# Performance work log

Hardware: AMD Instinct MI355X
Metric: run time of the kernel (lower is better)

## Reference

```python
import jax, jax.numpy as jnp
import numpy as np

N = 50000      # nodes
D = 256        # input_features
K = 64         # hiddens (per-head out dim)
H = 8          # nheads
O = 64         # outputs
E = 1600000    # edges
ALPHA = 0.2    # leaky-relu negative slope


def setup_inputs() -> dict:
    key = jax.random.key(0)
    ks = jax.random.split(key, 8)
    x = jax.random.normal(ks[0], (N, D), dtype=jnp.float32)
    edges = jax.random.randint(ks[1], (2, E), 0, N, dtype=jnp.int64)
    layer_W = jax.random.normal(ks[2], (D, D), dtype=jnp.float32) * (1.0 / np.sqrt(D))
    layer_b = jnp.zeros((D,), dtype=jnp.float32)
    heads_W = jax.random.normal(ks[3], (H, D, K), dtype=jnp.float32) * (1.0 / np.sqrt(D))
    heads_a = jax.random.normal(ks[4], (H, 2 * K), dtype=jnp.float32) * 0.1
    end_W = jax.random.normal(ks[5], (H * K, O), dtype=jnp.float32) * (1.0 / np.sqrt(H * K))
    end_a = jax.random.normal(ks[6], (2 * O,), dtype=jnp.float32) * 0.1
    return {"x": x, "edges": edges, "layer_W": layer_W, "layer_b": layer_b,
            "heads_W": heads_W, "heads_a": heads_a, "end_W": end_W, "end_a": end_a}


def _gat_layer(x, W, a, src, dst):
    # x: [N, Din], W: [Din, Dout], a: [2*Dout]
    h = x @ W                                    # [N, Dout]
    k = h.shape[1]
    # a . [h_src || h_dst] == (h @ a_src)[src] + (h @ a_dst)[dst]  (cheap: project then gather scalars)
    s = (h @ a[:k])[src] + (h @ a[k:])[dst]      # [E]
    e = jax.nn.leaky_relu(s, ALPHA)
    # numerically-stable segment softmax over edges grouped by destination node
    m = jax.ops.segment_max(e, dst, num_segments=N)        # [N]
    w = jnp.exp(e - m[dst])                                # [E]
    denom = jax.ops.segment_sum(w, dst, num_segments=N)    # [N]
    attn = w / (denom[dst] + 1e-16)                        # [E]
    out = jax.ops.segment_sum(attn[:, None] * h[src], dst, num_segments=N)  # [N, Dout]
    return jax.nn.elu(out)


def reference(x, edges, layer_W, layer_b, heads_W, heads_a, end_W, end_a):
    src, dst = edges[0], edges[1]
    x = x @ layer_W + layer_b                    # nn.Linear(input_features, input_features)
    # multi-head sparse attention, concat over heads -> [N, H*K]
    hcat = jnp.concatenate(
        [_gat_layer(x, heads_W[i], heads_a[i], src, dst) for i in range(H)], axis=1)
    out = _gat_layer(hcat, end_W, end_a, src, dst)  # [N, O]
    return jax.nn.softmax(out, axis=1)
```

## Files before the change

### kernel.cpp

```cpp
#include <hip/hip_runtime.h>
#include <hip/hip_fp16.h>
#include <math.h>

#define NN 50000
#define DD 256
#define KK 64
#define HH 8
#define OO 64
#define EE 1600000
#define LRELU_ALPHA 0.2f
#define HK 512
#define NX 640
#define N3 80

typedef __attribute__((ext_vector_type(8))) short short8;
typedef __attribute__((ext_vector_type(4))) float floatx4;
typedef __attribute__((ext_vector_type(4))) unsigned int uintx4;

__device__ inline void bsplit(float f, unsigned short& h, unsigned short& l) {
    unsigned u = __float_as_uint(f);
    h = (unsigned short)(u >> 16);
    float fh = __uint_as_float(u & 0xffff0000u);
    l = (unsigned short)(__float_as_uint(f - fh) >> 16);
}

__device__ inline void fmamix2(float& a0, float& a1, unsigned int pk, float w) {
    asm("v_fma_mix_f32 %0, %2, %3, %0 op_sel:[0,0,0] op_sel_hi:[1,0,0]\n\t"
        "v_fma_mix_f32 %1, %2, %3, %1 op_sel:[1,0,0] op_sel_hi:[1,0,0]"
        : "+v"(a0), "+v"(a1)
        : "v"(pk), "v"(w));
}

__global__ void pack_heads_kernel(const float* __restrict__ hw, float* __restrict__ Bp) {
    int t = blockIdx.x * 256 + threadIdx.x;
    if (t >= HH * DD * KK) return;
    int h = t >> 14;
    int r = t & 16383;
    int d = r >> 6;
    int k = r & 63;
    Bp[d * HK + h * KK + k] = hw[t];
}

__global__ void bias_pack_kernel(const float* __restrict__ b, const float* __restrict__ Bp,
                                 float* __restrict__ bc) {
    int c = blockIdx.x * 256 + threadIdx.x;
    if (c >= HK) return;
    float s = 0.f;
    for (int d = 0; d < DD; d++) s += b[d] * Bp[d * HK + c];
    bc[c] = s;
}

__global__ void build_wext_kernel(const float* __restrict__ Wc, const float* __restrict__ heads_a,
                                  unsigned short* __restrict__ Th, unsigned short* __restrict__ Tl) {
    int t = blockIdx.x * 256 + threadIdx.x;
    int col = t >> 8, d = t & 255;
    if (col >= NX) return;
    float v = 0.f;
    if (col < HK) {
        v = Wc[d * HK + col];
    } else if (col < HK + 8) {
        int h = col - HK;
        for (int k = 0; k < 64; k++) v += Wc[d * HK + h * 64 + k] * heads_a[h * 128 + k];
    } else if (col < HK + 16) {
        int h = col - HK - 8;
        for (int k = 0; k < 64; k++) v += Wc[d * HK + h * 64 + k] * heads_a[h * 128 + 64 + k];
    }
    unsigned short hi, lo;
    bsplit(v, hi, lo);
    Th[(size_t)col * DD + d] = hi;
    Tl[(size_t)col * DD + d] = lo;
}

__global__ void bias_ext_kernel(const float* __restrict__ bc, const float* __restrict__ heads_a,
                                float* __restrict__ be) {
    int c = blockIdx.x * 256 + threadIdx.x;
    if (c >= NX) return;
    float v = 0.f;
    if (c < HK) v = bc[c];
    else if (c < HK + 8) {
        int h = c - HK;
        for (int k = 0; k < 64; k++) v += bc[h * 64 + k] * heads_a[h * 128 + k];
    } else if (c < HK + 16) {
        int h = c - HK - 8;
        for (int k = 0; k < 64; k++) v += bc[h * 64 + k] * heads_a[h * 128 + 64 + k];
    }
    be[c] = v;
}

__global__ void build_eext_kernel(const float* __restrict__ eW, const float* __restrict__ ea,
                                  unsigned short* __restrict__ Th, unsigned short* __restrict__ Tl) {
    int t = blockIdx.x * 256 + threadIdx.x;
    int col = t >> 9, k = t & 511;
    if (col >= N3) return;
    float v = 0.f;
    if (col < OO) v = eW[(size_t)k * OO + col];
    else if (col == OO) { for (int j = 0; j < OO; j++) v += eW[(size_t)k * OO + j] * ea[j]; }
    else if (col == OO + 1) { for (int j = 0; j < OO; j++) v += eW[(size_t)k * OO + j] * ea[64 + j]; }
    unsigned short hi, lo;
    bsplit(v, hi, lo);
    Th[(size_t)col * HK + k] = hi;
    Tl[(size_t)col * HK + k] = lo;
}

__global__ void split_x_kernel(const float* __restrict__ x, unsigned short* __restrict__ xh,
                               unsigned short* __restrict__ xl) {
    int t = blockIdx.x * 256 + threadIdx.x;
    if (t >= NN * 64) return;
    float4 v = ((const float4*)x)[t];
    ushort4 vh, vl;
    bsplit(v.x, vh.x, vl.x);
    bsplit(v.y, vh.y, vl.y);
    bsplit(v.z, vh.z, vl.z);
    bsplit(v.w, vh.w, vl.w);
    ((ushort4*)xh)[t] = vh;
    ((ushort4*)xl)[t] = vl;
}

#define GM 128
#define GN 128
#define GKT 16
__global__ __launch_bounds__(256) void sgemm128_kernel(
    const float* __restrict__ A, const float* __restrict__ B,
    const float* __restrict__ bias, float* __restrict__ C,
    int M, int N, int K)
{
    __shared__ float As[GKT][GM + 4];
    __shared__ float Bs[GKT][GN + 4];
    int tid = threadIdx.x;
    int row0 = blockIdx.y * GM, col0 = blockIdx.x * GN;
    int tx = tid & 15, ty = tid >> 4;
    int ar = tid >> 1;
    int ac0 = (tid & 1) * 8;
    float acc[8][8] = {};
    for (int k0 = 0; k0 < K; k0 += GKT) {
#pragma unroll
        for (int i = 0; i < 2; i++) {
            int gr = row0 + ar;
            int gc = k0 + ac0 + i * 4;
            float4 v = make_float4(0.f, 0.f, 0.f, 0.f);
            if (gr < M) v = *(const float4*)&A[(size_t)gr * K + gc];
            As[ac0 + i * 4 + 0][ar] = v.x;
            As[ac0 + i * 4 + 1][ar] = v.y;
            As[ac0 + i * 4 + 2][ar] = v.z;
            As[ac0 + i * 4 + 3][ar] = v.w;
        }
#pragma unroll
        for (int i = 0; i < 2; i++) {
            int idx = tid + i * 256;
            int br = idx >> 5;
            int bc = (idx & 31) * 4;
            float4 v = make_float4(0.f, 0.f, 0.f, 0.f);
            int gc = col0 + bc;
            if (gc < N) v = *(const float4*)&B[(size_t)(k0 + br) * N + gc];
            *(float4*)&Bs[br][bc] = v;
        }
        __syncthreads();
#pragma unroll
        for (int k = 0; k < GKT; k++) {
            float4 a0 = *(const float4*)&As[k][ty * 4];
            float4 a1 = *(const float4*)&As[k][64 + ty * 4];
            float4 b0 = *(const float4*)&Bs[k][tx * 4];
            float4 b1 = *(const float4*)&Bs[k][64 + tx * 4];
            float av[8] = {a0.x, a0.y, a0.z, a0.w, a1.x, a1.y, a1.z, a1.w};
            float bv[8] = {b0.x, b0.y, b0.z, b0.w, b1.x, b1.y, b1.z, b1.w};
#pragma unroll
            for (int i = 0; i < 8; i++)
#pragma unroll
                for (int j = 0; j < 8; j++) acc[i][j] += av[i] * bv[j];
        }
        __syncthreads();
    }
#pragma unroll
    for (int i = 0; i < 8; i++) {
        int gr = row0 + (i < 4 ? ty * 4 + i : 64 + ty * 4 + i - 4);
        if (gr >= M) continue;
#pragma unroll
        for (int j = 0; j < 8; j++) {
            int gc = col0 + (j < 4 ? tx * 4 + j : 64 + tx * 4 + j - 4);
            if (gc >= N) continue;
            float v = acc[i][j];
            if (bias) v += bias[gc];
            C[(size_t)gr * N + gc] = v;
        }
    }
}

#define LDA 40
__global__ __launch_bounds__(256) void mfma_gemm1_kernel(
    const unsigned short* __restrict__ xh, const unsigned short* __restrict__ xl,
    const unsigned short* __restrict__ BhT, const unsigned short* __restrict__ BlT,
    const float* __restrict__ bias_ext,
    __half* __restrict__ Hh, float* __restrict__ ssrc_n, float* __restrict__ sdst_n)
{
    __shared__ unsigned short AhL[128 * LDA];
    __shared__ unsigned short AlL[128 * LDA];
    __shared__ unsigned short BhL[128 * LDA];
    __shared__ unsigned short BlL[128 * LDA];
    int tid = threadIdx.x, widx = tid >> 6, lane = tid & 63;
    int row0 = blockIdx.y * 128, col0 = blockIdx.x * 128;
    int wrow = (widx >> 1) * 64, wcol = (widx & 1) * 64;
    int lrow = lane & 15, lq = lane >> 4;
    int sr = tid >> 1;
    int sc = (tid & 1) * 16;
    int gr = row0 + sr;
    size_t abase = (gr < NN) ? (size_t)gr * DD : 0;
    size_t bbase = (size_t)(col0 + sr) * DD;
    floatx4 acc[4][4] = {};
    uint4 pah0, pah1, pal0, pal1, pbh0, pbh1, pbl0, pbl1;
    {
        size_t ab = abase + sc, bb = bbase + sc;
        pah0 = *(const uint4*)&xh[ab];   pah1 = *(const uint4*)&xh[ab + 8];
        pal0 = *(const uint4*)&xl[ab];   pal1 = *(const uint4*)&xl[ab + 8];
        pbh0 = *(const uint4*)&BhT[bb];  pbh1 = *(const uint4*)&BhT[bb + 8];
        pbl0 = *(const uint4*)&BlT[bb];  pbl1 = *(const uint4*)&BlT[bb + 8];
    }
    for (int k0 = 0; k0 < DD; k0 += 32) {
        *(uint4*)&AhL[sr * LDA + sc]     = pah0;
        *(uint4*)&AhL[sr * LDA + sc + 8] = pah1;
        *(uint4*)&AlL[sr * LDA + sc]     = pal0;
        *(uint4*)&AlL[sr * LDA + sc + 8] = pal1;
        *(uint4*)&BhL[sr * LDA + sc]     = pbh0;
        *(uint4*)&BhL[sr * LDA + sc + 8] = pbh1;
        *(uint4*)&BlL[sr * LDA + sc]     = pbl0;
        *(uint4*)&BlL[sr * LDA + sc + 8] = pbl1;
        __syncthreads();
        if (k0 + 32 < DD) {
            size_t ab = abase + k0 + 32 + sc, bb = bbase + k0 + 32 + sc;
            pah0 = *(const uint4*)&xh[ab];   pah1 = *(const uint4*)&xh[ab + 8];
            pal0 = *(const uint4*)&xl[ab];   pal1 = *(const uint4*)&xl[ab + 8];
            pbh0 = *(const uint4*)&BhT[bb];  pbh1 = *(const uint4*)&BhT[bb + 8];
            pbl0 = *(const uint4*)&BlT[bb];  pbl1 = *(const uint4*)&BlT[bb + 8];
        }
        short8 ah[4], al[4], bh[4], bl[4];
#pragma unroll
        for (int mi = 0; mi < 4; mi++) {
            int r = wrow + mi * 16 + lrow;
            ah[mi] = *(const short8*)&AhL[r * LDA + lq * 8];
            al[mi] = *(const short8*)&AlL[r * LDA + lq * 8];
        }
#pragma unroll
        for (int ni = 0; ni < 4; ni++) {
            int c = wcol + ni * 16 + lrow;
            bh[ni] = *(const short8*)&BhL[c * LDA + lq * 8];
            bl[ni] = *(const short8*)&BlL[c * LDA + lq * 8];
        }
#pragma unroll
        for (int mi = 0; mi < 4; mi++)
#pragma unroll
            for (int ni = 0; ni < 4; ni++) {
                acc[mi][ni] = __builtin_amdgcn_mfma_f32_16x16x32_bf16(al[mi], bh[ni], acc[mi][ni], 0, 0, 0);
                acc[mi][ni] = __builtin_amdgcn_mfma_f32_16x16x32_bf16(ah[mi], bl[ni], acc[mi][ni], 0, 0, 0);
                acc[mi][ni] = __builtin_amdgcn_mfma_f32_16x16x32_bf16(ah[mi], bh[ni], acc[mi][ni], 0, 0, 0);
            }
        __syncthreads();
    }
#pragma unroll
    for (int mi = 0; mi < 4; mi++)
#pragma unroll
        for (int ni = 0; ni < 4; ni++)
#pragma unroll
            for (int r = 0; r < 4; r++) {
                int grow = row0 + wrow + mi * 16 + lq * 4 + r;
                int gcol = col0 + wcol + ni * 16 + lrow;
                if (grow < NN && gcol < HK + 16) {
                    float v = acc[mi][ni][r] + bias_ext[gcol];
                    if (gcol < HK)
                        Hh[(size_t)grow * HK + gcol] = __float2half_rn(v);
                    else if (gcol < HK + 8)
                        ssrc_n[(size_t)grow * 8 + (gcol - HK)] = v;
                    else
                        sdst_n[(size_t)grow * 8 + (gcol - HK - 8)] = v;
                }
            }
}

__global__ __launch_bounds__(256) void mfma_gemm3_kernel(
    const unsigned short* __restrict__ hch, const unsigned short* __restrict__ hcl,
    const unsigned short* __restrict__ BhT, const unsigned short* __restrict__ BlT,
    __half* __restrict__ h2, float* __restrict__ s2src, float* __restrict__ s2dst)
{
    __shared__ unsigned short AhL[64 * LDA];
    __shared__ unsigned short AlL[64 * LDA];
    __shared__ unsigned short BhL[N3 * LDA];
    __shared__ unsigned short BlL[N3 * LDA];
    int tid = threadIdx.x, widx = tid >> 6, lane = tid & 63;
    int row0 = blockIdx.x * 64;
    int wrow = widx * 16;
    int lrow = lane & 15, lq = lane >> 4;
    int sr = tid >> 2;
    int sc = (tid & 3) * 8;
    int gr = row0 + sr;
    size_t abase = (gr < NN) ? (size_t)gr * HK : 0;
    int bidx0 = tid;
    int br0 = bidx0 >> 2, bc0 = (bidx0 & 3) * 8;
    int bidx1 = tid + 256;
    bool b1ok = (bidx1 < N3 * 4);
    int br1 = bidx1 >> 2, bc1 = (bidx1 & 3) * 8;
    floatx4 acc[5] = {};
    uint4 pa0, pa1, pb0h, pb0l, pb1h, pb1l;
    {
        pa0 = *(const uint4*)&hch[abase + sc];
        pa1 = *(const uint4*)&hcl[abase + sc];
        pb0h = *(const uint4*)&BhT[(size_t)br0 * HK + bc0];
        pb0l = *(const uint4*)&BlT[(size_t)br0 * HK + bc0];
        if (b1ok) {
            pb1h = *(const uint4*)&BhT[(size_t)br1 * HK + bc1];
            pb1l = *(const uint4*)&BlT[(size_t)br1 * HK + bc1];
        }
    }
    for (int k0 = 0; k0 < HK; k0 += 32) {
        *(uint4*)&AhL[sr * LDA + sc] = pa0;
        *(uint4*)&AlL[sr * LDA + sc] = pa1;
        *(uint4*)&BhL[br0 * LDA + bc0] = pb0h;
        *(uint4*)&BlL[br0 * LDA + bc0] = pb0l;
        if (b1ok) {
            *(uint4*)&BhL[br1 * LDA + bc1] = pb1h;
            *(uint4*)&BlL[br1 * LDA + bc1] = pb1l;
        }
        __syncthreads();
        if (k0 + 32 < HK) {
            size_t ab = abase + k0 + 32 + sc;
            pa0 = *(const uint4*)&hch[ab];
            pa1 = *(const uint4*)&hcl[ab];
            pb0h = *(const uint4*)&BhT[(size_t)br0 * HK + k0 + 32 + bc0];
            pb0l = *(const uint4*)&BlT[(size_t)br0 * HK + k0 + 32 + bc0];
            if (b1ok) {
                pb1h = *(const uint4*)&BhT[(size_t)br1 * HK + k0 + 32 + bc1];
                pb1l = *(const uint4*)&BlT[(size_t)br1 * HK + k0 + 32 + bc1];
            }
        }
        short8 ah, al, bh[5], bl[5];
        int r = wrow + lrow;
        ah = *(const short8*)&AhL[r * LDA + lq * 8];
        al = *(const short8*)&AlL[r * LDA + lq * 8];
#pragma unroll
        for (int ni = 0; ni < 5; ni++) {
            int c = ni * 16 + lrow;
            bh[ni] = *(const short8*)&BhL[c * LDA + lq * 8];
            bl[ni] = *(const short8*)&BlL[c * LDA + lq * 8];
        }
#pragma unroll
        for (int ni = 0; ni < 5; ni++) {
            acc[ni] = __builtin_amdgcn_mfma_f32_16x16x32_bf16(al, bh[ni], acc[ni], 0, 0, 0);
            acc[ni] = __builtin_amdgcn_mfma_f32_16x16x32_bf16(ah, bl[ni], acc[ni], 0, 0, 0);
            acc[ni] = __builtin_amdgcn_mfma_f32_16x16x32_bf16(ah, bh[ni], acc[ni], 0, 0, 0);
        }
        __syncthreads();
    }
#pragma unroll
    for (int ni = 0; ni < 5; ni++)
#pragma unroll
        for (int r = 0; r < 4; r++) {
            int grow = row0 + wrow + lq * 4 + r;
            int gcol = ni * 16 + lrow;
            if (grow < NN) {
                float v = acc[ni][r];
                if (gcol < OO) h2[(size_t)grow * OO + gcol] = __float2half_rn(v);
                else if (gcol == OO) s2src[grow] = v;
                else if (gcol == OO + 1) s2dst[grow] = v;
            }
        }
}

__global__ void hist_kernel(const int* __restrict__ dst, int* __restrict__ deg) {
    int t = blockIdx.x * 256 + threadIdx.x;
    if (t < EE) atomicAdd(&deg[dst[t]], 1);
}

__global__ void scan1_kernel(const int* __restrict__ deg, int* __restrict__ part,
                             int* __restrict__ bsum) {
    __shared__ int ws_[4];
    int i = blockIdx.x * 256 + threadIdx.x;
    int lane = threadIdx.x & 63, wv = threadIdx.x >> 6;
    int v = (i < NN) ? deg[i] : 0;
    int x = v;
#pragma unroll
    for (int d = 1; d < 64; d <<= 1) {
        int t = __shfl_up(x, d, 64);
        if (lane >= d) x += t;
    }
    if (lane == 63) ws_[wv] = x;
    __syncthreads();
    int add = 0;
    for (int k = 0; k < wv; k++) add += ws_[k];
    x += add;
    if (i < NN) part[i] = x;
    if (threadIdx.x == 255) bsum[blockIdx.x] = x;
}

__global__ void scan2_kernel(int* __restrict__ bsum, int nb) {
    __shared__ int ws_[4];
    int tid = threadIdx.x;
    int lane = tid & 63, wv = tid >> 6;
    int v = (tid < nb) ? bsum[tid] : 0;
    int x = v;
#pragma unroll
    for (int d = 1; d < 64; d <<= 1) {
        int t = __shfl_up(x, d, 64);
        if (lane >= d) x += t;
    }
    if (lane == 63) ws_[wv] = x;
    __syncthreads();
    int add = 0;
    for (int k = 0; k < wv; k++) add += ws_[k];
    x += add;
    if (tid < nb) bsum[tid] = x;
}

__global__ void scan3_kernel(const int* __restrict__ deg, const int* __restrict__ part,
                             const int* __restrict__ bsum, int* __restrict__ offs,
                             int* __restrict__ cursor) {
    int i = blockIdx.x * 256 + threadIdx.x;
    if (i >= NN) return;
    int carry = blockIdx.x ? bsum[blockIdx.x - 1] : 0;
    int incl = part[i] + carry;
    offs[i + 1] = incl;
    cursor[i] = incl - deg[i];
    if (i == 0) offs[0] = 0;
}

__global__ void scatter_kernel(const int* __restrict__ src, const int* __restrict__ dst,
                               int* __restrict__ cursor, int* __restrict__ ssorted) {
    int t = blockIdx.x * 256 + threadIdx.x;
    if (t < EE) {
        int d = dst[t];
        int pos = atomicAdd(&cursor[d], 1);
        ssorted[pos] = src[t];
    }
}

#define APE 4
__global__ __launch_bounds__(256) void agg_heads_kernel(
    const __half* __restrict__ Hh, const float* __restrict__ ssrc_n,
    const float* __restrict__ sdst_n, const int* __restrict__ offs,
    const int* __restrict__ ssorted,
    unsigned short* __restrict__ hch, unsigned short* __restrict__ hcl)
{
    __shared__ int2 sSW[4][64];
    int wv = threadIdx.x >> 6, lane = threadIdx.x & 63;
    int n = blockIdx.x * 4 + wv;
    if (n >= NN) return;
    int beg = offs[n], deg = offs[n + 1] - beg;
    int eg = lane >> 3, hh = lane & 7;
    float acc[8] = {};
    float den = 0.f;
    float sd = sdst_n[(size_t)n * 8 + hh];
    for (int c0 = 0; c0 < deg; c0 += 8) {
        int jj = c0 + eg;
        int s = 0;
        float wgt = 0.f;
        if (jj < deg) {
            s = ssorted[beg + jj];
            float sv = ssrc_n[(size_t)s * 8 + hh] + sd;
            float e = (sv >= 0.f) ? sv : LRELU_ALPHA * sv;
            wgt = __expf(e);
        }
        den += wgt;
        sSW[wv][lane] = make_int2(s, __float_as_int(wgt));
        int ec = min(8, deg - c0);
#pragma unroll
        for (int base = 0; base < 8; base += APE) {
            if (base >= ec) break;
            uint4 vb[APE];
            float wb[APE];
#pragma unroll
            for (int p = 0; p < APE; p++) {
                int2 t2 = sSW[wv][(base + p) * 8 + (lane >> 3)];
                wb[p] = __int_as_float(t2.y);
                vb[p] = *(const uint4*)&Hh[((size_t)t2.x << 9) + lane * 8];
            }
#pragma unroll
            for (int p = 0; p < APE; p++) {
                fmamix2(acc[0], acc[1], vb[p].x, wb[p]);
                fmamix2(acc[2], acc[3], vb[p].y, wb[p]);
                fmamix2(acc[4], acc[5], vb[p].z, wb[p]);
                fmamix2(acc[6], acc[7], vb[p].w, wb[p]);
            }
        }
    }
    den += __shfl_xor(den, 8, 64);
    den += __shfl_xor(den, 16, 64);
    den += __shfl_xor(den, 32, 64);
    float denf = __shfl(den, lane >> 3, 64);
    float inv = 1.f / (denf + 1e-16f);
    unsigned int phw[4], plw[4];
#pragma unroll
    for (int j = 0; j < 4; j++) {
        float r0 = acc[2 * j] * inv, r1 = acc[2 * j + 1] * inv;
        r0 = (r0 > 0.f) ? r0 : (__expf(r0) - 1.f);
        r1 = (r1 > 0.f) ? r1 : (__expf(r1) - 1.f);
        unsigned short h0, l0, h1, l1;
        bsplit(r0, h0, l0);
        bsplit(r1, h1, l1);
        phw[j] = (unsigned)h0 | ((unsigned)h1 << 16);
        plw[j] = (unsigned)l0 | ((unsigned)l1 << 16);
    }
    size_t o = (size_t)n * HK + lane * 8;
    uintx4 vph, vpl;
    vph.x = phw[0]; vph.y = phw[1]; vph.z = phw[2]; vph.w = phw[3];
    vpl.x = plw[0]; vpl.y = plw[1]; vpl.z = plw[2]; vpl.w = plw[3];
    __builtin_nontemporal_store(vph, (uintx4*)&hch[o]);
    __builtin_nontemporal_store(vpl, (uintx4*)&hcl[o]);
}

#define APW 4
__global__ __launch_bounds__(256) void agg_final_kernel(
    const __half* __restrict__ h2, const float* __restrict__ s2src,
    const float* __restrict__ s2dst, const int* __restrict__ offs,
    const int* __restrict__ ssorted, float* __restrict__ out)
{
    __shared__ int2 sSW[4][64];
    int wv = threadIdx.x >> 6, lane = threadIdx.x & 63;
    int n = blockIdx.x * 4 + wv;
    if (n >= NN) return;
    int beg = offs[n], deg = offs[n + 1] - beg;
    int g = lane >> 3, q = lane & 7;
    float acc[8] = {};
    float den = 0.f;
    float sd = (deg > 0) ? s2dst[n] : 0.f;
    for (int c0 = 0; c0 < deg; c0 += 64) {
        int jj = c0 + lane;
        int s = 0;
        float wgt = 0.f;
        if (jj < deg) {
            s = ssorted[beg + jj];
            float sv = s2src[s] + sd;
            float e = (sv >= 0.f) ? sv : LRELU_ALPHA * sv;
            wgt = __expf(e);
        }
        den += wgt;
        sSW[wv][lane] = make_int2(s, __float_as_int(wgt));
        int clen = min(64, deg - c0);
        int nst = (clen + 7) >> 3;
        for (int base = 0; base < nst; base += APW) {
            uint4 vb[APW];
            float wb[APW];
#pragma unroll
            for (int p2 = 0; p2 < APW; p2++) {
                int st = base + p2;
                int sj = 0;
                float ww = 0.f;
                if (st < nst) {
                    int2 t2 = sSW[wv][st * 8 + g];
                    sj = t2.x;
                    ww = __int_as_float(t2.y);
                }
                wb[p2] = ww;
                vb[p2] = *(const uint4*)&h2[(size_t)sj * OO + q * 8];
            }
#pragma unroll
            for (int p2 = 0; p2 < APW; p2++) {
                fmamix2(acc[0], acc[1], vb[p2].x, wb[p2]);
                fmamix2(acc[2], acc[3], vb[p2].y, wb[p2]);
                fmamix2(acc[4], acc[5], vb[p2].z, wb[p2]);
                fmamix2(acc[6], acc[7], vb[p2].w, wb[p2]);
            }
        }
    }
#pragma unroll
    for (int off = 32; off; off >>= 1) den += __shfl_xor(den, off, 64);
#pragma unroll
    for (int f = 0; f < 8; f++) {
        acc[f] += __shfl_xor(acc[f], 8, 64);
        acc[f] += __shfl_xor(acc[f], 16, 64);
        acc[f] += __shfl_xor(acc[f], 32, 64);
    }
    float inv = 1.f / (den + 1e-16f);
    float r[8];
#pragma unroll
    for (int f = 0; f < 8; f++) {
        float v = acc[f] * inv;
        r[f] = (v > 0.f) ? v : (__expf(v) - 1.f);
    }
    float mm = r[0];
#pragma unroll
    for (int f = 1; f < 8; f++) mm = fmaxf(mm, r[f]);
#pragma unroll
    for (int off = 1; off < 8; off <<= 1) mm = fmaxf(mm, __shfl_xor(mm, off, 64));
    float p[8], sum = 0.f;
#pragma unroll
    for (int f = 0; f < 8; f++) { p[f] = __expf(r[f] - mm); sum += p[f]; }
#pragma unroll
    for (int off = 1; off < 8; off <<= 1) sum += __shfl_xor(sum, off, 64);
    float is = 1.f / sum;
    if (g == 0) {
        float4 o0 = make_float4(p[0] * is, p[1] * is, p[2] * is, p[3] * is);
        float4 o1 = make_float4(p[4] * is, p[5] * is, p[6] * is, p[7] * is);
        *(float4*)&out[(size_t)n * OO + q * 8] = o0;
        *(float4*)&out[(size_t)n * OO + q * 8 + 4] = o1;
    }
}

extern "C" void kernel_launch(void* const* d_in, const int* in_sizes, int n_in,
                              void* d_out, int out_size, void* d_ws, size_t ws_size,
                              hipStream_t stream) {
    const float* x       = (const float*)d_in[0];
    const int*   edges   = (const int*)d_in[1];
    const float* layer_W = (const float*)d_in[2];
    const float* layer_b = (const float*)d_in[3];
    const float* heads_W = (const float*)d_in[4];
    const float* heads_a = (const float*)d_in[5];
    const float* end_W   = (const float*)d_in[6];
    const float* end_a   = (const float*)d_in[7];
    float* out = (float*)d_out;

    const int* src = edges;
    const int* dst = edges + EE;

    char* ws = (char*)d_ws;
    size_t wsp = 0;
    auto alloc = [&](size_t bytes) -> void* {
        void* r = ws + wsp;
        wsp += (bytes + 255) & ~(size_t)255;
        return r;
    };
    __half* Hh    = (__half*)alloc((size_t)NN * HK * 2);
    unsigned short* hch = (unsigned short*)alloc((size_t)NN * HK * 2);
    unsigned short* hcl = (unsigned short*)alloc((size_t)NN * HK * 2);
    __half* h2    = (__half*)alloc((size_t)NN * OO * 2);
    float* Bp    = (float*)alloc((size_t)DD * HK * 4);
    float* Wc    = (float*)alloc((size_t)DD * HK * 4);
    float* bc    = (float*)alloc((size_t)HK * 4);
    unsigned short* WexthT = (unsigned short*)alloc((size_t)NX * DD * 2);
    unsigned short* WextlT = (unsigned short*)alloc((size_t)NX * DD * 2);
    unsigned short* eexthT = (unsigned short*)alloc((size_t)N3 * HK * 2);
    unsigned short* eextlT = (unsigned short*)alloc((size_t)N3 * HK * 2);
    float* bias_ext = (float*)alloc((size_t)NX * 4);
    float* ssrc_n = (float*)alloc((size_t)NN * 8 * 4);
    float* sdst_n = (float*)alloc((size_t)NN * 8 * 4);
    float* s2src = (float*)alloc((size_t)NN * 4);
    float* s2dst = (float*)alloc((size_t)NN * 4);
    int* deg     = (int*)alloc((size_t)NN * 4);
    int* offs    = (int*)alloc((size_t)(NN + 1) * 4);
    int* cursor  = (int*)alloc((size_t)NN * 4);
    int* part    = (int*)alloc((size_t)NN * 4);
    int* bsum    = (int*)alloc((size_t)256 * 4);
    int* ssorted = (int*)alloc((size_t)EE * 4);

    unsigned short* xh = hch;
    unsigned short* xl = hcl;

    const int NB = (NN + 255) / 256;

    (void)hipMemsetAsync(deg, 0, (size_t)NN * 4, stream);

    pack_heads_kernel<<<(HH * DD * KK + 255) / 256, 256, 0, stream>>>(heads_W, Bp);
    bias_pack_kernel<<<2, 256, 0, stream>>>(layer_b, Bp, bc);
    sgemm128_kernel<<<dim3(HK / GN, DD / GM), 256, 0, stream>>>(
        layer_W, Bp, nullptr, Wc, DD, HK, DD);
    build_wext_kernel<<<(NX * DD + 255) / 256, 256, 0, stream>>>(Wc, heads_a, WexthT, WextlT);
    bias_ext_kernel<<<(NX + 255) / 256, 256, 0, stream>>>(bc, heads_a, bias_ext);
    build_eext_kernel<<<(N3 * HK + 255) / 256, 256, 0, stream>>>(end_W, end_a, eexthT, eextlT);
    split_x_kernel<<<(NN * 64 + 255) / 256, 256, 0, stream>>>(x, xh, xl);

    mfma_gemm1_kernel<<<dim3(NX / 128, (NN + 127) / 128), 256, 0, stream>>>(
        xh, xl, WexthT, WextlT, bias_ext, Hh, ssrc_n, sdst_n);

    hist_kernel<<<(EE + 255) / 256, 256, 0, stream>>>(dst, deg);
    scan1_kernel<<<NB, 256, 0, stream>>>(deg, part, bsum);
    scan2_kernel<<<1, 256, 0, stream>>>(bsum, NB);
    scan3_kernel<<<NB, 256, 0, stream>>>(deg, part, bsum, offs, cursor);
    scatter_kernel<<<(EE + 255) / 256, 256, 0, stream>>>(src, dst, cursor, ssorted);

    agg_heads_kernel<<<(NN + 3) / 4, 256, 0, stream>>>(
        Hh, ssrc_n, sdst_n, offs, ssorted, hch, hcl);

    mfma_gemm3_kernel<<<(NN + 63) / 64, 256, 0, stream>>>(
        hch, hcl, eexthT, eextlT, h2, s2src, s2dst);

    agg_final_kernel<<<(NN + 3) / 4, 256, 0, stream>>>(h2, s2src, s2dst, offs, ssorted, out);
}
```

Baseline: 802.5 us.

## Split head aggregation into head-pair passes with head-group-major feature layout

GEMM1 now writes the per-head features in a head-pair-major layout, [4 groups][N][2 heads][64]. The head aggregation kernel launches four times as many blocks, each covering one head pair, so each gathered source row is a contiguous 256-byte chunk. The working set per pass is smaller, which is meant to improve cache hit rates on the random gathers. In exchange, the CSR offsets, indices and softmax scores are re-read four times, and cross-lane shuffle reductions are added over the four edge sub-groups, which do redundant work.

After: 780.4 us. 1.03x faster.

```diff
diff --git a/kernel.cpp b/kernel.cpp
--- a/kernel.cpp
+++ b/kernel.cpp
@@ -12,6 +12,7 @@
 #define HK 512
 #define NX 640
 #define N3 80
+#define NGB 12500
 
 typedef __attribute__((ext_vector_type(8))) short short8;
 typedef __attribute__((ext_vector_type(4))) float floatx4;
@@ -190,7 +191,7 @@
     const unsigned short* __restrict__ xh, const unsigned short* __restrict__ xl,
     const unsigned short* __restrict__ BhT, const unsigned short* __restrict__ BlT,
     const float* __restrict__ bias_ext,
-    __half* __restrict__ Hh, float* __restrict__ ssrc_n, float* __restrict__ sdst_n)
+    __half* __restrict__ Hh2, float* __restrict__ ssrc_n, float* __restrict__ sdst_n)
 {
     __shared__ unsigned short AhL[128 * LDA];
     __shared__ unsigned short AlL[128 * LDA];
@@ -264,9 +265,11 @@
                 int gcol = col0 + wcol + ni * 16 + lrow;
                 if (grow < NN && gcol < HK + 16) {
                     float v = acc[mi][ni][r] + bias_ext[gcol];
-                    if (gcol < HK)
-                        Hh[(size_t)grow * HK + gcol] = __float2half_rn(v);
-                    else if (gcol < HK + 8)
+                    if (gcol < HK) {
+                        int h = gcol >> 6, k = gcol & 63;
+                        int hg = h >> 1, h2 = h & 1;
+                        Hh2[(((size_t)hg * NN + grow) * 2 + h2) * 64 + k] = __float2half_rn(v);
+                    } else if (gcol < HK + 8)
                         ssrc_n[(size_t)grow * 8 + (gcol - HK)] = v;
                     else
                         sdst_n[(size_t)grow * 8 + (gcol - HK - 8)] = v;
@@ -429,48 +432,51 @@
     }
 }
 
-#define APE 4
+#define APE2 4
 __global__ __launch_bounds__(256) void agg_heads_kernel(
-    const __half* __restrict__ Hh, const float* __restrict__ ssrc_n,
+    const __half* __restrict__ Hh2, const float* __restrict__ ssrc_n,
     const float* __restrict__ sdst_n, const int* __restrict__ offs,
     const int* __restrict__ ssorted,
     unsigned short* __restrict__ hch, unsigned short* __restrict__ hcl)
 {
     __shared__ int2 sSW[4][64];
     int wv = threadIdx.x >> 6, lane = threadIdx.x & 63;
-    int n = blockIdx.x * 4 + wv;
+    int hg = blockIdx.x / NGB;
+    int ng = blockIdx.x - hg * NGB;
+    int n = ng * 4 + wv;
     if (n >= NN) return;
     int beg = offs[n], deg = offs[n + 1] - beg;
-    int eg = lane >> 3, hh = lane & 7;
+    int se = lane >> 1, sh = lane & 1;
+    int lidx16 = lane & 15;
+    const __half* Hs = Hh2 + (size_t)hg * NN * 128;
+    float sd = sdst_n[(size_t)n * 8 + hg * 2 + sh];
     float acc[8] = {};
     float den = 0.f;
-    float sd = sdst_n[(size_t)n * 8 + hh];
-    for (int c0 = 0; c0 < deg; c0 += 8) {
-        int jj = c0 + eg;
+    for (int c0 = 0; c0 < deg; c0 += 32) {
+        int jj = c0 + se;
         int s = 0;
         float wgt = 0.f;
         if (jj < deg) {
             s = ssorted[beg + jj];
-            float sv = ssrc_n[(size_t)s * 8 + hh] + sd;
+            float sv = ssrc_n[(size_t)s * 8 + hg * 2 + sh] + sd;
             float e = (sv >= 0.f) ? sv : LRELU_ALPHA * sv;
             wgt = __expf(e);
         }
         den += wgt;
         sSW[wv][lane] = make_int2(s, __float_as_int(wgt));
-        int ec = min(8, deg - c0);
-#pragma unroll
-        for (int base = 0; base < 8; base += APE) {
-            if (base >= ec) break;
-            uint4 vb[APE];
-            float wb[APE];
-#pragma unroll
-            for (int p = 0; p < APE; p++) {
-                int2 t2 = sSW[wv][(base + p) * 8 + (lane >> 3)];
+        int ec = min(32, deg - c0);
+        for (int base = 0; base < ec; base += 16) {
+            uint4 vb[APE2];
+            float wb[APE2];
+#pragma unroll
+            for (int p = 0; p < APE2; p++) {
+                int e = base + p * 4 + (lane >> 4);
+                int2 t2 = sSW[wv][e * 2 + ((lane >> 3) & 1)];
                 wb[p] = __int_as_float(t2.y);
-                vb[p] = *(const uint4*)&Hh[((size_t)t2.x << 9) + lane * 8];
-            }
-#pragma unroll
-            for (int p = 0; p < APE; p++) {
+                vb[p] = *(const uint4*)&Hs[(size_t)t2.x * 128 + lidx16 * 8];
+            }
+#pragma unroll
+            for (int p = 0; p < APE2; p++) {
                 fmamix2(acc[0], acc[1], vb[p].x, wb[p]);
                 fmamix2(acc[2], acc[3], vb[p].y, wb[p]);
                 fmamix2(acc[4], acc[5], vb[p].z, wb[p]);
@@ -478,29 +484,38 @@
             }
         }
     }
+    den += __shfl_xor(den, 2, 64);
+    den += __shfl_xor(den, 4, 64);
     den += __shfl_xor(den, 8, 64);
     den += __shfl_xor(den, 16, 64);
     den += __shfl_xor(den, 32, 64);
-    float denf = __shfl(den, lane >> 3, 64);
-    float inv = 1.f / (denf + 1e-16f);
-    unsigned int phw[4], plw[4];
-#pragma unroll
-    for (int j = 0; j < 4; j++) {
-        float r0 = acc[2 * j] * inv, r1 = acc[2 * j + 1] * inv;
-        r0 = (r0 > 0.f) ? r0 : (__expf(r0) - 1.f);
-        r1 = (r1 > 0.f) ? r1 : (__expf(r1) - 1.f);
-        unsigned short h0, l0, h1, l1;
-        bsplit(r0, h0, l0);
-        bsplit(r1, h1, l1);
-        phw[j] = (unsigned)h0 | ((unsigned)h1 << 16);
-        plw[j] = (unsigned)l0 | ((unsigned)l1 << 16);
-    }
-    size_t o = (size_t)n * HK + lane * 8;
-    uintx4 vph, vpl;
-    vph.x = phw[0]; vph.y = phw[1]; vph.z = phw[2]; vph.w = phw[3];
-    vpl.x = plw[0]; vpl.y = plw[1]; vpl.z = plw[2]; vpl.w = plw[3];
-    __builtin_nontemporal_store(vph, (uintx4*)&hch[o]);
-    __builtin_nontemporal_store(vpl, (uintx4*)&hcl[o]);
+    float denf = __shfl(den, (lane >> 3) & 1, 64);
+#pragma unroll
+    for (int f = 0; f < 8; f++) {
+        acc[f] += __shfl_xor(acc[f], 16, 64);
+        acc[f] += __shfl_xor(acc[f], 32, 64);
+    }
+    if (lane < 16) {
+        float inv = 1.f / (denf + 1e-16f);
+        unsigned int phw[4], plw[4];
+#pragma unroll
+        for (int j = 0; j < 4; j++) {
+            float r0 = acc[2 * j] * inv, r1 = acc[2 * j + 1] * inv;
+            r0 = (r0 > 0.f) ? r0 : (__expf(r0) - 1.f);
+            r1 = (r1 > 0.f) ? r1 : (__expf(r1) - 1.f);
+            unsigned short h0, l0, h1, l1;
+            bsplit(r0, h0, l0);
+            bsplit(r1, h1, l1);
+            phw[j] = (unsigned)h0 | ((unsigned)h1 << 16);
+            plw[j] = (unsigned)l0 | ((unsigned)l1 << 16);
+        }
+        size_t o = (size_t)n * HK + hg * 128 + lidx16 * 8;
+        uintx4 vph, vpl;
+        vph.x = phw[0]; vph.y = phw[1]; vph.z = phw[2]; vph.w = phw[3];
+        vpl.x = plw[0]; vpl.y = plw[1]; vpl.z = plw[2]; vpl.w = plw[3];
+        __builtin_nontemporal_store(vph, (uintx4*)&hch[o]);
+        __builtin_nontemporal_store(vpl, (uintx4*)&hcl[o]);
+    }
 }
 
 #define APW 4
@@ -614,7 +629,7 @@
         wsp += (bytes + 255) & ~(size_t)255;
         return r;
     };
-    __half* Hh    = (__half*)alloc((size_t)NN * HK * 2);
+    __half* Hh2   = (__half*)alloc((size_t)NN * HK * 2);
     unsigned short* hch = (unsigned short*)alloc((size_t)NN * HK * 2);
     unsigned short* hcl = (unsigned short*)alloc((size_t)NN * HK * 2);
     __half* h2    = (__half*)alloc((size_t)NN * OO * 2);
@@ -654,7 +669,7 @@
     split_x_kernel<<<(NN * 64 + 255) / 256, 256, 0, stream>>>(x, xh, xl);
 
     mfma_gemm1_kernel<<<dim3(NX / 128, (NN + 127) / 128), 256, 0, stream>>>(
-        xh, xl, WexthT, WextlT, bias_ext, Hh, ssrc_n, sdst_n);
+        xh, xl, WexthT, WextlT, bias_ext, Hh2, ssrc_n, sdst_n);
 
     hist_kernel<<<(EE + 255) / 256, 256, 0, stream>>>(dst, deg);
     scan1_kernel<<<NB, 256, 0, stream>>>(deg, part, bsum);
@@ -662,8 +677,8 @@
     scan3_kernel<<<NB, 256, 0, stream>>>(deg, part, bsum, offs, cursor);
     scatter_kernel<<<(EE + 255) / 256, 256, 0, stream>>>(src, dst, cursor, ssorted);
 
-    agg_heads_kernel<<<(NN + 3) / 4, 256, 0, stream>>>(
-        Hh, ssrc_n, sdst_n, offs, ssorted, hch, hcl);
+    agg_heads_kernel<<<4 * NGB, 256, 0, stream>>>(
+        Hh2, ssrc_n, sdst_n, offs, ssorted, hch, hcl);
 
     mfma_gemm3_kernel<<<(NN + 63) / 64, 256, 0, stream>>>(
         hch, hcl, eexthT, eextlT, h2, s2src, s2dst);
```
